# Kernel tuning notes

Hardware: AMD Instinct MI355X
Metric: run time of the kernel (lower is better)

The kernel has to match this reference:

```python
import jax, jax.numpy as jnp
import numpy as np

WS = (7, 7, 7)          # window size (s, h, w)
N_TOK = WS[0] * WS[1] * WS[2]   # 343
DIM = 96
HEADS = 3
N_WINDOWS = 64
BATCH = 8
B_ = BATCH * N_WINDOWS  # 512


def _rel_pos_index(ws):
    s, h, w = ws
    coords = np.stack(np.meshgrid(np.arange(s), np.arange(h), np.arange(w), indexing='ij'))
    cf = coords.reshape(3, -1)                     # [3, N]
    rel = cf[:, :, None] - cf[:, None, :]          # [3, N, N]
    rel = rel.transpose(1, 2, 0).astype(np.int64)  # [N, N, 3]
    rel[..., 0] += s - 1
    rel[..., 1] += h - 1
    rel[..., 2] += w - 1
    rel[..., 0] *= (2 * h - 1) * (2 * w - 1)
    rel[..., 1] *= (2 * w - 1)
    return rel.sum(-1)                             # [N, N] in [0, (2s-1)(2h-1)(2w-1))


def setup_inputs() -> dict:
    key = jax.random.key(0)
    ks = jax.random.split(key, 8)
    table_len = (2 * WS[0] - 1) * (2 * WS[1] - 1) * (2 * WS[2] - 1)  # 2197
    return {
        'x': jax.random.normal(ks[0], (B_, N_TOK, DIM), dtype=jnp.float32),
        'mask': jax.random.normal(ks[1], (N_WINDOWS, N_TOK, N_TOK), dtype=jnp.float32),
        'qkv_w': jax.random.normal(ks[2], (3 * DIM, DIM), dtype=jnp.float32) * 0.02,
        'qkv_b': jax.random.normal(ks[3], (3 * DIM,), dtype=jnp.float32) * 0.02,
        'proj_w': jax.random.normal(ks[4], (DIM, DIM), dtype=jnp.float32) * 0.02,
        'proj_b': jax.random.normal(ks[5], (DIM,), dtype=jnp.float32) * 0.02,
        'rpb_table': jax.random.normal(ks[6], (table_len, HEADS), dtype=jnp.float32) * 0.02,
        'rel_index': jnp.asarray(_rel_pos_index(WS), dtype=jnp.int32),
    }


def reference(x, mask, qkv_w, qkv_b, proj_w, proj_b, rpb_table, rel_index):
    B, N, C = x.shape
    H = rpb_table.shape[1]
    hd = C // H
    scale = hd ** -0.5

    qkv = x @ qkv_w.T + qkv_b                         # [B, N, 3C]
    qkv = qkv.reshape(B, N, 3, H, hd).transpose(2, 0, 3, 1, 4)  # [3, B, H, N, hd]
    q, k, v = qkv[0] * scale, qkv[1], qkv[2]

    attn = jnp.einsum('bhnd,bhmd->bhnm', q, k)        # [B, H, N, N]
    bias = rpb_table[rel_index].transpose(2, 0, 1)    # [H, N, N]
    attn = attn + bias[None]

    nW = mask.shape[0]
    attn = attn.reshape(B // nW, nW, H, N, N) + mask[None, :, None]
    attn = jax.nn.softmax(attn.reshape(B, H, N, N), axis=-1)

    out = jnp.einsum('bhnm,bhmd->bnhd', attn, v).reshape(B, N, C)
    return out @ proj_w.T + proj_b
```

## Files before the change

### kernel.cpp

```cpp
#include <hip/hip_runtime.h>
#include <stdint.h>

#define NTOK 343
#define L2E 1.4426950408889634f
#define SCALE (0.17677669529663687f * 1.4426950408889634f)

typedef uint32_t u32a __attribute__((may_alias));
typedef __attribute__((ext_vector_type(8))) short short8;
typedef short8 bfrag __attribute__((may_alias));
typedef __attribute__((ext_vector_type(4))) float f32x4;
typedef f32x4 f32x4a __attribute__((may_alias));
typedef __attribute__((ext_vector_type(2))) uint32_t u32x2;
typedef u32x2 u32x2a __attribute__((may_alias));

static __device__ __forceinline__ uint16_t f2bf(float f) {
    uint32_t u = __float_as_uint(f);
    u += 0x7fffu + ((u >> 16) & 1u);
    return (uint16_t)(u >> 16);
}
static __device__ __forceinline__ float bflo(uint32_t p) { return __uint_as_float(p << 16); }
static __device__ __forceinline__ float bfhi(uint32_t p) { return __uint_as_float(p & 0xffff0000u); }

static __device__ __forceinline__ float exp2_fast(float x) {
    float r;
    __asm__("v_exp_f32 %0, %1" : "=v"(r) : "v"(x));
    return r;
}
static __device__ __forceinline__ uint32_t cvtpk_bf16(float lo, float hi) {
    uint32_t r;
    __asm__("v_cvt_pk_bf16_f32 %0, %1, %2" : "=v"(r) : "v"(lo), "v"(hi));
    return r;
}

union abits { uint32_t u[4]; bfrag f; };

__global__ __launch_bounds__(256) void comb_pre(const float* __restrict__ mask,
                                                const float* __restrict__ rpb,
                                                const int* __restrict__ rel,
                                                u32a* __restrict__ comb) {
    int e = blockIdx.x * 256 + threadIdx.x;
    const int total = 64 * NTOK * 176;
    if (e >= total) return;
    int m16 = e & 15;
    int tp = (e >> 4) % 11;
    int rest = e / 176;
    int i = rest % NTOK;
    int w = rest / NTOK;
    int j0 = tp * 32 + m16;
    int j1 = j0 + 16;
    const float* mrow = mask + ((size_t)w * NTOK + i) * NTOK;
    const int* rrow = rel + i * NTOK;
    float mk0 = mrow[j0];
    int r0 = rrow[j0] * 3;
    const bool ok1 = (j1 < NTOK);
    float mk1 = ok1 ? mrow[j1] : 0.f;
    int r1 = ok1 ? rrow[j1] * 3 : 0;
    u32a* cbase = comb + ((size_t)(w * 3) * NTOK + i) * 176 + tp * 16 + m16;
    #pragma unroll
    for (int h = 0; h < 3; ++h) {
        float c0 = (mk0 + rpb[r0 + h]) * L2E;
        uint32_t hi = 0xFF80u;
        if (ok1) hi = (uint32_t)f2bf((mk1 + rpb[r1 + h]) * L2E);
        cbase[(size_t)h * (NTOK * 176)] = (uint32_t)f2bf(c0) | (hi << 16);
    }
}

__global__ __launch_bounds__(256, 2) void qkv_kernel(
    const float* __restrict__ x, const float* __restrict__ qkv_w,
    const float* __restrict__ qkv_b,
    uint16_t* __restrict__ q_ws, uint16_t* __restrict__ k_ws, uint16_t* __restrict__ v_ws)
{
    __shared__ uint16_t w_l[288 * 104];
    __shared__ __align__(16) float bias_l[288];
    const int tid = threadIdx.x;

    {
        f32x4 tmp[27];
        #pragma unroll
        for (int i = 0; i < 27; ++i)
            tmp[i] = ((const f32x4a*)qkv_w)[tid + i * 256];
        for (int e = tid; e < 288; e += 256) {
            float bb = qkv_b[e];
            bias_l[e] = (e < 96) ? bb * SCALE : bb;
        }
        #pragma unroll
        for (int i = 0; i < 27; ++i) {
            int c4 = tid + i * 256;
            int c = c4 / 24, k = (c4 - c * 24) * 4;
            f32x4 v = tmp[i];
            float s = (c < 96) ? SCALE : 1.f;
            uint32_t lo = cvtpk_bf16(v[0] * s, v[1] * s);
            uint32_t hi = cvtpk_bf16(v[2] * s, v[3] * s);
            u32x2 pk = {lo, hi};
            *(u32x2a*)(w_l + c * 104 + k) = pk;
        }
    }
    __syncthreads();

    const int lane = tid & 63, wv4 = tid >> 6;
    const int m = lane & 15, quad = lane >> 4;

    f32x4 bs4[18];
    #pragma unroll
    for (int ct = 0; ct < 18; ++ct)
        bs4[ct] = *(const f32x4*)(bias_l + ct * 16 + 4 * quad);

    uint16_t* const dsts[3] = {q_ws, k_ws, v_ws};
    const int rowbase_blk = blockIdx.x * 256;

    for (int it = 0; it < 4; ++it) {
        const int rowbase = rowbase_blk + (wv4 * 4 + it) * 16;
        const int row = rowbase + m;
        const float* xr = x + (size_t)row * 96;
        abits A[3];
        #pragma unroll
        for (int ch = 0; ch < 3; ++ch) {
            f32x4 a0 = *(const f32x4a*)(xr + ch * 32 + quad * 8);
            f32x4 a1 = *(const f32x4a*)(xr + ch * 32 + quad * 8 + 4);
            A[ch].u[0] = cvtpk_bf16(a0[0], a0[1]);
            A[ch].u[1] = cvtpk_bf16(a0[2], a0[3]);
            A[ch].u[2] = cvtpk_bf16(a1[0], a1[1]);
            A[ch].u[3] = cvtpk_bf16(a1[2], a1[3]);
        }

        f32x4 C[18];
        #pragma unroll
        for (int ct = 0; ct < 18; ++ct) C[ct] = (f32x4){0.f, 0.f, 0.f, 0.f};

        #pragma unroll
        for (int ch = 0; ch < 3; ++ch) {
            #pragma unroll
            for (int ct = 0; ct < 18; ++ct) {
                bfrag bf_ = *(const bfrag*)(w_l + (ct * 16 + m) * 104 + ch * 32 + quad * 8);
                C[ct] = __builtin_amdgcn_mfma_f32_16x16x32_bf16(bf_, A[ch].f, C[ct], 0, 0, 0);
            }
        }

        const int bb = row / 343;
        const int nn = row - bb * 343;
        #pragma unroll
        for (int ct = 0; ct < 18; ++ct) {
            const int sel = ct / 6;
            const int base = (ct % 6) * 16 + 4 * quad;
            const int hd = base >> 5, dd = base & 31;
            f32x4 vv = C[ct] + bs4[ct];
            uint32_t lo = cvtpk_bf16(vv[0], vv[1]);
            uint32_t hi = cvtpk_bf16(vv[2], vv[3]);
            uint16_t* dp_ = dsts[sel] + ((size_t)(bb * 3 + hd) * NTOK + nn) * 32 + dd;
            u32x2 pk = {lo, hi};
            *(u32x2a*)dp_ = pk;
        }
    }
}

__global__ __launch_bounds__(256, 2) void attn_kernel(
    uint16_t* __restrict__ q_ws, const uint16_t* __restrict__ k_ws,
    const uint16_t* __restrict__ v_ws, const u32a* __restrict__ comb)
{
    __shared__ uint16_t k_l[352 * 40];
    __shared__ uint16_t vT[32 * 360];
    __shared__ uint16_t pstage[4][16 * 104];

    const int bh = blockIdx.x;
    const int b = bh / 3, h = bh - b * 3, w = b & 63;
    const int tid = threadIdx.x, lane = tid & 63, wv = tid >> 6;
    const int m = lane & 15, quad = lane >> 4;
    const int wh = w * 3 + h;

    const u32a* ksrc = (const u32a*)(k_ws + (size_t)bh * NTOK * 32);
    const u32a* vsrc = (const u32a*)(v_ws + (size_t)bh * NTOK * 32);
    u32a* k32 = (u32a*)k_l;
    {
        uint32_t tk[22], tv[22];
        #pragma unroll
        for (int i = 0; i < 22; ++i) {
            int e = tid + i * 256;
            if (e < NTOK * 16) { tk[i] = ksrc[e]; tv[i] = vsrc[e]; }
        }
        #pragma unroll
        for (int i = 0; i < 22; ++i) {
            int e = tid + i * 256;
            if (e < NTOK * 16) {
                int tok = e >> 4, dp = e & 15;
                k32[tok * 20 + dp] = tk[i];
                uint32_t vv = tv[i];
                int kp = ((tok >> 5) << 5) + ((tok & 15) << 1) + ((tok >> 4) & 1);
                vT[(2 * dp) * 360 + kp]     = (uint16_t)(vv & 0xffffu);
                vT[(2 * dp + 1) * 360 + kp] = (uint16_t)(vv >> 16);
            }
        }
    }
    for (int e = tid; e < 9 * 16; e += 256) {
        int tok = 343 + (e >> 4), dp = e & 15;
        k32[tok * 20 + dp] = 0;
    }
    for (int e = tid; e < 32 * 9; e += 256) {
        int d = e / 9, tok = 343 + (e % 9);
        int kp = ((tok >> 5) << 5) + ((tok & 15) << 1) + ((tok >> 4) & 1);
        vT[d * 360 + kp] = 0;
    }
    __syncthreads();

    uint16_t* qbase = q_ws + (size_t)bh * NTOK * 32;
    uint16_t* stg = pstage[wv];

    for (int ti = wv; ti < 22; ti += 4) {
        const int i0 = ti * 16;
        bfrag qf = *(const bfrag*)(qbase + (size_t)(i0 + m) * 32 + quad * 8);
        uint32_t cw[4][11];
        #pragma unroll
        for (int r = 0; r < 4; ++r) {
            int ir = i0 + 4 * quad + r;
            ir = (ir > 342) ? 342 : ir;
            const u32a* crow = comb + ((size_t)(wh * NTOK + ir)) * 176 + m;
            #pragma unroll
            for (int tp = 0; tp < 11; ++tp)
                cw[r][tp] = crow[tp * 16];
        }

        f32x4 S[22];
        #pragma unroll
        for (int t = 0; t < 22; ++t) S[t] = (f32x4){0.f, 0.f, 0.f, 0.f};
        __builtin_amdgcn_s_setprio(1);
        #pragma unroll
        for (int t = 0; t < 22; ++t) {
            bfrag kf = *(const bfrag*)(k_l + (t * 16 + m) * 40 + quad * 8);
            S[t] = __builtin_amdgcn_mfma_f32_16x16x32_bf16(qf, kf, S[t], 0, 0, 0);
        }
        __builtin_amdgcn_s_setprio(0);

        float sum[4] = {0.f, 0.f, 0.f, 0.f};

        f32x4 O0 = (f32x4){0.f, 0.f, 0.f, 0.f};
        f32x4 O1 = (f32x4){0.f, 0.f, 0.f, 0.f};
        #pragma unroll
        for (int qt = 0; qt < 4; ++qt) {
            const int nch = (qt == 3) ? 2 : 3;
            #pragma unroll
            for (int uu = 0; uu < 3; ++uu) {
                if (uu < nch) {
                    const int tp = qt * 3 + uu;
                    #pragma unroll
                    for (int r = 0; r < 4; ++r) {
                        float e0 = exp2_fast(S[2 * tp][r] + bflo(cw[r][tp]));
                        float e1 = exp2_fast(S[2 * tp + 1][r] + bfhi(cw[r][tp]));
                        sum[r] += e0 + e1;
                        *(u32a*)(stg + (4 * quad + r) * 104 + uu * 32 + 2 * m) =
                            cvtpk_bf16(e0, e1);
                    }
                }
            }
            __asm__ __volatile__("" ::: "memory");
            __builtin_amdgcn_s_waitcnt(0xC07F);
            __asm__ __volatile__("" ::: "memory");

            __builtin_amdgcn_s_setprio(1);
            #pragma unroll
            for (int c = 0; c < 3; ++c) {
                if (c < nch) {
                    const int jj = qt * 96 + c * 32;
                    bfrag pf = *(const bfrag*)(stg + m * 104 + c * 32 + quad * 8);
                    bfrag v0 = *(const bfrag*)(vT + (size_t)m * 360 + jj + quad * 8);
                    bfrag v1 = *(const bfrag*)(vT + (size_t)(m + 16) * 360 + jj + quad * 8);
                    O0 = __builtin_amdgcn_mfma_f32_16x16x32_bf16(pf, v0, O0, 0, 0, 0);
                    O1 = __builtin_amdgcn_mfma_f32_16x16x32_bf16(pf, v1, O1, 0, 0, 0);
                }
            }
            __builtin_amdgcn_s_setprio(0);
            __asm__ __volatile__("" ::: "memory");
        }

        float inv_[4];
        #pragma unroll
        for (int r = 0; r < 4; ++r) {
            float v = sum[r];
            v += __shfl_xor(v, 1);
            v += __shfl_xor(v, 2);
            v += __shfl_xor(v, 4);
            v += __shfl_xor(v, 8);
            inv_[r] = 1.f / v;
        }

        #pragma unroll
        for (int r = 0; r < 4; ++r) {
            const int ir = i0 + 4 * quad + r;
            if (ir < NTOK) {
                uint16_t* orow = qbase + (size_t)ir * 32;
                orow[m]      = f2bf(O0[r] * inv_[r]);
                orow[m + 16] = f2bf(O1[r] * inv_[r]);
            }
        }
    }
}

__global__ __launch_bounds__(256) void proj_kernel(
    const uint16_t* __restrict__ ao, const float* __restrict__ proj_w,
    const float* __restrict__ proj_b, float* __restrict__ out)
{
    __shared__ uint16_t w_l[96 * 104];
    const int tid = threadIdx.x;
    {
        f32x4 tmp[9];
        #pragma unroll
        for (int i = 0; i < 9; ++i)
            tmp[i] = ((const f32x4a*)proj_w)[tid + i * 256];
        #pragma unroll
        for (int i = 0; i < 9; ++i) {
            int c4 = tid + i * 256;
            int c = c4 / 24, k = (c4 - c * 24) * 4;
            f32x4 v = tmp[i];
            uint32_t lo = cvtpk_bf16(v[0], v[1]);
            uint32_t hi = cvtpk_bf16(v[2], v[3]);
            u32x2 pk = {lo, hi};
            *(u32x2a*)(w_l + c * 104 + k) = pk;
        }
    }
    __syncthreads();

    const int lane = tid & 63, wv4 = tid >> 6;
    const int m = lane & 15, quad = lane >> 4;

    float bp[6];
    #pragma unroll
    for (int ct = 0; ct < 6; ++ct) bp[ct] = proj_b[ct * 16 + m];

    const int rowbase_blk = blockIdx.x * 256;

    for (int it = 0; it < 4; ++it) {
        const int rowbase = rowbase_blk + (wv4 * 4 + it) * 16;
        const int rm = rowbase + m;
        const int bm = rm / 343;
        const int nm = rm - bm * 343;

        f32x4 C[6];
        #pragma unroll
        for (int ct = 0; ct < 6; ++ct) C[ct] = (f32x4){0.f, 0.f, 0.f, 0.f};

        #pragma unroll
        for (int ch = 0; ch < 3; ++ch) {
            bfrag af = *(const bfrag*)(ao + ((size_t)(bm * 3 + ch) * NTOK + nm) * 32 + quad * 8);
            #pragma unroll
            for (int ct = 0; ct < 6; ++ct) {
                bfrag bf_ = *(const bfrag*)(w_l + (ct * 16 + m) * 104 + ch * 32 + quad * 8);
                C[ct] = __builtin_amdgcn_mfma_f32_16x16x32_bf16(af, bf_, C[ct], 0, 0, 0);
            }
        }

        #pragma unroll
        for (int r = 0; r < 4; ++r) {
            const int rr = rowbase + 4 * quad + r;
            #pragma unroll
            for (int ct = 0; ct < 6; ++ct)
                out[(size_t)rr * 96 + ct * 16 + m] = C[ct][r] + bp[ct];
        }
    }
}

extern "C" void kernel_launch(void* const* d_in, const int* in_sizes, int n_in,
                              void* d_out, int out_size, void* d_ws, size_t ws_size,
                              hipStream_t stream) {
    const float* x      = (const float*)d_in[0];
    const float* mask   = (const float*)d_in[1];
    const float* qkv_w  = (const float*)d_in[2];
    const float* qkv_b  = (const float*)d_in[3];
    const float* proj_w = (const float*)d_in[4];
    const float* proj_b = (const float*)d_in[5];
    const float* rpb    = (const float*)d_in[6];
    const int*   rel    = (const int*)d_in[7];
    float* out = (float*)d_out;

    uint16_t* q_ws = (uint16_t*)d_ws;
    uint16_t* k_ws = q_ws + 16859136;
    uint16_t* v_ws = k_ws + 16859136;
    u32a* comb = (u32a*)((char*)d_ws + 101154816);

    const int comb_total = 64 * NTOK * 176;
    comb_pre<<<dim3((comb_total + 255) / 256), 256, 0, stream>>>(mask, rpb, rel, comb);
    qkv_kernel<<<dim3(686), 256, 0, stream>>>(x, qkv_w, qkv_b, q_ws, k_ws, v_ws);
    attn_kernel<<<dim3(512 * 3), 256, 0, stream>>>(q_ws, k_ws, v_ws, comb);
    proj_kernel<<<dim3(686), 256, 0, stream>>>(q_ws, proj_w, proj_b, out);
}
```

Measured before the change: 330.3 us.

## Restructure QKV and projection GEMM kernels for load prefetch and fewer accumulators

```diff
diff --git a/kernel.cpp b/kernel.cpp
--- a/kernel.cpp
+++ b/kernel.cpp
@@ -65,7 +65,55 @@
     }
 }
 
-__global__ __launch_bounds__(256, 2) void qkv_kernel(
+#define QKV_LOADX(DST, ROW) do { \
+    const float* xr_ = x + (size_t)(ROW) * 96 + quad * 8; \
+    DST##0 = *(const f32x4a*)(xr_); \
+    DST##1 = *(const f32x4a*)(xr_ + 4); \
+    DST##2 = *(const f32x4a*)(xr_ + 32); \
+    DST##3 = *(const f32x4a*)(xr_ + 36); \
+    DST##4 = *(const f32x4a*)(xr_ + 64); \
+    DST##5 = *(const f32x4a*)(xr_ + 68); \
+} while (0)
+
+#define QKV_COMPUTE(SRC, ITC) do { \
+    abits A0_, A1_, A2_; \
+    A0_.u[0] = cvtpk_bf16(SRC##0[0], SRC##0[1]); \
+    A0_.u[1] = cvtpk_bf16(SRC##0[2], SRC##0[3]); \
+    A0_.u[2] = cvtpk_bf16(SRC##1[0], SRC##1[1]); \
+    A0_.u[3] = cvtpk_bf16(SRC##1[2], SRC##1[3]); \
+    A1_.u[0] = cvtpk_bf16(SRC##2[0], SRC##2[1]); \
+    A1_.u[1] = cvtpk_bf16(SRC##2[2], SRC##2[3]); \
+    A1_.u[2] = cvtpk_bf16(SRC##3[0], SRC##3[1]); \
+    A1_.u[3] = cvtpk_bf16(SRC##3[2], SRC##3[3]); \
+    A2_.u[0] = cvtpk_bf16(SRC##4[0], SRC##4[1]); \
+    A2_.u[1] = cvtpk_bf16(SRC##4[2], SRC##4[3]); \
+    A2_.u[2] = cvtpk_bf16(SRC##5[0], SRC##5[1]); \
+    A2_.u[3] = cvtpk_bf16(SRC##5[2], SRC##5[3]); \
+    const int rowc = row0 + (ITC) * 16; \
+    const int bbc = rowc / 343; \
+    const int nnc = rowc - bbc * 343; \
+    _Pragma("unroll") \
+    for (int ct = 0; ct < 18; ++ct) { \
+        f32x4 Cl = (f32x4){0.f, 0.f, 0.f, 0.f}; \
+        bfrag w0_ = *(const bfrag*)(w_l + (ct * 16 + m) * 104 + quad * 8); \
+        Cl = __builtin_amdgcn_mfma_f32_16x16x32_bf16(w0_, A0_.f, Cl, 0, 0, 0); \
+        bfrag w1_ = *(const bfrag*)(w_l + (ct * 16 + m) * 104 + 32 + quad * 8); \
+        Cl = __builtin_amdgcn_mfma_f32_16x16x32_bf16(w1_, A1_.f, Cl, 0, 0, 0); \
+        bfrag w2_ = *(const bfrag*)(w_l + (ct * 16 + m) * 104 + 64 + quad * 8); \
+        Cl = __builtin_amdgcn_mfma_f32_16x16x32_bf16(w2_, A2_.f, Cl, 0, 0, 0); \
+        f32x4 b4_ = *(const f32x4*)(bias_l + ct * 16 + 4 * quad); \
+        f32x4 vv_ = Cl + b4_; \
+        const int sel_ = ct / 6; \
+        const int base_ = (ct % 6) * 16 + 4 * quad; \
+        const int hd_ = base_ >> 5, dd_ = base_ & 31; \
+        uint32_t lo_ = cvtpk_bf16(vv_[0], vv_[1]); \
+        uint32_t hi_ = cvtpk_bf16(vv_[2], vv_[3]); \
+        u32x2 pk_ = {lo_, hi_}; \
+        *(u32x2a*)(dsts[sel_] + ((size_t)(bbc * 3 + hd_) * NTOK + nnc) * 32 + dd_) = pk_; \
+    } \
+} while (0)
+
+__global__ __launch_bounds__(512, 4) void qkv_kernel(
     const float* __restrict__ x, const float* __restrict__ qkv_w,
     const float* __restrict__ qkv_b,
     uint16_t* __restrict__ q_ws, uint16_t* __restrict__ k_ws, uint16_t* __restrict__ v_ws)
@@ -75,82 +123,44 @@
     const int tid = threadIdx.x;
 
     {
-        f32x4 tmp[27];
-        #pragma unroll
-        for (int i = 0; i < 27; ++i)
-            tmp[i] = ((const f32x4a*)qkv_w)[tid + i * 256];
-        for (int e = tid; e < 288; e += 256) {
+        f32x4 tmp[14];
+        #pragma unroll
+        for (int i = 0; i < 14; ++i) {
+            int idx = tid + i * 512;
+            if (idx < 6912) tmp[i] = ((const f32x4a*)qkv_w)[idx];
+        }
+        for (int e = tid; e < 288; e += 512) {
             float bb = qkv_b[e];
             bias_l[e] = (e < 96) ? bb * SCALE : bb;
         }
         #pragma unroll
-        for (int i = 0; i < 27; ++i) {
-            int c4 = tid + i * 256;
-            int c = c4 / 24, k = (c4 - c * 24) * 4;
-            f32x4 v = tmp[i];
-            float s = (c < 96) ? SCALE : 1.f;
-            uint32_t lo = cvtpk_bf16(v[0] * s, v[1] * s);
-            uint32_t hi = cvtpk_bf16(v[2] * s, v[3] * s);
-            u32x2 pk = {lo, hi};
-            *(u32x2a*)(w_l + c * 104 + k) = pk;
+        for (int i = 0; i < 14; ++i) {
+            int idx = tid + i * 512;
+            if (idx < 6912) {
+                int c = idx / 24, k = (idx - c * 24) * 4;
+                f32x4 v = tmp[i];
+                float s = (c < 96) ? SCALE : 1.f;
+                uint32_t lo = cvtpk_bf16(v[0] * s, v[1] * s);
+                uint32_t hi = cvtpk_bf16(v[2] * s, v[3] * s);
+                u32x2 pk = {lo, hi};
+                *(u32x2a*)(w_l + c * 104 + k) = pk;
+            }
         }
     }
     __syncthreads();
 
-    const int lane = tid & 63, wv4 = tid >> 6;
+    const int lane = tid & 63, wv8 = tid >> 6;
     const int m = lane & 15, quad = lane >> 4;
 
-    f32x4 bs4[18];
-    #pragma unroll
-    for (int ct = 0; ct < 18; ++ct)
-        bs4[ct] = *(const f32x4*)(bias_l + ct * 16 + 4 * quad);
-
     uint16_t* const dsts[3] = {q_ws, k_ws, v_ws};
-    const int rowbase_blk = blockIdx.x * 256;
-
-    for (int it = 0; it < 4; ++it) {
-        const int rowbase = rowbase_blk + (wv4 * 4 + it) * 16;
-        const int row = rowbase + m;
-        const float* xr = x + (size_t)row * 96;
-        abits A[3];
-        #pragma unroll
-        for (int ch = 0; ch < 3; ++ch) {
-            f32x4 a0 = *(const f32x4a*)(xr + ch * 32 + quad * 8);
-            f32x4 a1 = *(const f32x4a*)(xr + ch * 32 + quad * 8 + 4);
-            A[ch].u[0] = cvtpk_bf16(a0[0], a0[1]);
-            A[ch].u[1] = cvtpk_bf16(a0[2], a0[3]);
-            A[ch].u[2] = cvtpk_bf16(a1[0], a1[1]);
-            A[ch].u[3] = cvtpk_bf16(a1[2], a1[3]);
-        }
-
-        f32x4 C[18];
-        #pragma unroll
-        for (int ct = 0; ct < 18; ++ct) C[ct] = (f32x4){0.f, 0.f, 0.f, 0.f};
-
-        #pragma unroll
-        for (int ch = 0; ch < 3; ++ch) {
-            #pragma unroll
-            for (int ct = 0; ct < 18; ++ct) {
-                bfrag bf_ = *(const bfrag*)(w_l + (ct * 16 + m) * 104 + ch * 32 + quad * 8);
-                C[ct] = __builtin_amdgcn_mfma_f32_16x16x32_bf16(bf_, A[ch].f, C[ct], 0, 0, 0);
-            }
-        }
-
-        const int bb = row / 343;
-        const int nn = row - bb * 343;
-        #pragma unroll
-        for (int ct = 0; ct < 18; ++ct) {
-            const int sel = ct / 6;
-            const int base = (ct % 6) * 16 + 4 * quad;
-            const int hd = base >> 5, dd = base & 31;
-            f32x4 vv = C[ct] + bs4[ct];
-            uint32_t lo = cvtpk_bf16(vv[0], vv[1]);
-            uint32_t hi = cvtpk_bf16(vv[2], vv[3]);
-            uint16_t* dp_ = dsts[sel] + ((size_t)(bb * 3 + hd) * NTOK + nn) * 32 + dd;
-            u32x2 pk = {lo, hi};
-            *(u32x2a*)dp_ = pk;
-        }
-    }
+    const int row0 = blockIdx.x * 256 + wv8 * 32 + m;
+
+    f32x4 tA0, tA1, tA2, tA3, tA4, tA5;
+    f32x4 tB0, tB1, tB2, tB3, tB4, tB5;
+    QKV_LOADX(tA, row0);
+    QKV_LOADX(tB, row0 + 16);
+    QKV_COMPUTE(tA, 0);
+    QKV_COMPUTE(tB, 1);
 }
 
 __global__ __launch_bounds__(256, 2) void attn_kernel(
@@ -293,6 +303,30 @@
     }
 }
 
+#define PROJ_LOADA(DST, RM) do { \
+    const int bm_ = (RM) / 343; \
+    const int nm_ = (RM) - bm_ * 343; \
+    const uint16_t* ab_ = ao + ((size_t)(bm_ * 3) * NTOK + nm_) * 32 + quad * 8; \
+    DST##0 = *(const bfrag*)(ab_); \
+    DST##1 = *(const bfrag*)(ab_ + (size_t)NTOK * 32); \
+    DST##2 = *(const bfrag*)(ab_ + (size_t)(2 * NTOK) * 32); \
+} while (0)
+
+#define PROJ_COMPUTE(SRC, ITC) do { \
+    float* orow_ = out + (size_t)(row0 + (ITC) * 16) * 96 + 4 * quad; \
+    _Pragma("unroll") \
+    for (int ct = 0; ct < 6; ++ct) { \
+        f32x4 Cl = (f32x4){0.f, 0.f, 0.f, 0.f}; \
+        bfrag w0_ = *(const bfrag*)(w_l + (ct * 16 + m) * 104 + quad * 8); \
+        Cl = __builtin_amdgcn_mfma_f32_16x16x32_bf16(w0_, SRC##0, Cl, 0, 0, 0); \
+        bfrag w1_ = *(const bfrag*)(w_l + (ct * 16 + m) * 104 + 32 + quad * 8); \
+        Cl = __builtin_amdgcn_mfma_f32_16x16x32_bf16(w1_, SRC##1, Cl, 0, 0, 0); \
+        bfrag w2_ = *(const bfrag*)(w_l + (ct * 16 + m) * 104 + 64 + quad * 8); \
+        Cl = __builtin_amdgcn_mfma_f32_16x16x32_bf16(w2_, SRC##2, Cl, 0, 0, 0); \
+        *(f32x4a*)(orow_ + ct * 16) = Cl + bp4[ct]; \
+    } \
+} while (0)
+
 __global__ __launch_bounds__(256) void proj_kernel(
     const uint16_t* __restrict__ ao, const float* __restrict__ proj_w,
     const float* __restrict__ proj_b, float* __restrict__ out)
@@ -320,40 +354,22 @@
     const int lane = tid & 63, wv4 = tid >> 6;
     const int m = lane & 15, quad = lane >> 4;
 
-    float bp[6];
+    f32x4 bp4[6];
     #pragma unroll
-    for (int ct = 0; ct < 6; ++ct) bp[ct] = proj_b[ct * 16 + m];
-
-    const int rowbase_blk = blockIdx.x * 256;
-
-    for (int it = 0; it < 4; ++it) {
-        const int rowbase = rowbase_blk + (wv4 * 4 + it) * 16;
-        const int rm = rowbase + m;
-        const int bm = rm / 343;
-        const int nm = rm - bm * 343;
-
-        f32x4 C[6];
-        #pragma unroll
-        for (int ct = 0; ct < 6; ++ct) C[ct] = (f32x4){0.f, 0.f, 0.f, 0.f};
-
-        #pragma unroll
-        for (int ch = 0; ch < 3; ++ch) {
-            bfrag af = *(const bfrag*)(ao + ((size_t)(bm * 3 + ch) * NTOK + nm) * 32 + quad * 8);
-            #pragma unroll
-            for (int ct = 0; ct < 6; ++ct) {
-                bfrag bf_ = *(const bfrag*)(w_l + (ct * 16 + m) * 104 + ch * 32 + quad * 8);
-                C[ct] = __builtin_amdgcn_mfma_f32_16x16x32_bf16(af, bf_, C[ct], 0, 0, 0);
-            }
-        }
-
-        #pragma unroll
-        for (int r = 0; r < 4; ++r) {
-            const int rr = rowbase + 4 * quad + r;
-            #pragma unroll
-            for (int ct = 0; ct < 6; ++ct)
-                out[(size_t)rr * 96 + ct * 16 + m] = C[ct][r] + bp[ct];
-        }
-    }
+    for (int ct = 0; ct < 6; ++ct)
+        bp4[ct] = *(const f32x4a*)(proj_b + ct * 16 + 4 * quad);
+
+    const int row0 = blockIdx.x * 256 + wv4 * 64 + m;
+
+    bfrag aA0, aA1, aA2, aB0, aB1, aB2;
+    PROJ_LOADA(aA, row0);
+    PROJ_LOADA(aB, row0 + 16);
+    PROJ_COMPUTE(aA, 0);
+    PROJ_LOADA(aA, row0 + 32);
+    PROJ_COMPUTE(aB, 1);
+    PROJ_LOADA(aB, row0 + 48);
+    PROJ_COMPUTE(aA, 2);
+    PROJ_COMPUTE(aB, 3);
 }
 
 extern "C" void kernel_launch(void* const* d_in, const int* in_sizes, int n_in,
@@ -376,7 +392,7 @@
 
     const int comb_total = 64 * NTOK * 176;
     comb_pre<<<dim3((comb_total + 255) / 256), 256, 0, stream>>>(mask, rpb, rel, comb);
-    qkv_kernel<<<dim3(686), 256, 0, stream>>>(x, qkv_w, qkv_b, q_ws, k_ws, v_ws);
+    qkv_kernel<<<dim3(686), 512, 0, stream>>>(x, qkv_w, qkv_b, q_ws, k_ws, v_ws);
     attn_kernel<<<dim3(512 * 3), 256, 0, stream>>>(q_ws, k_ws, v_ws, comb);
     proj_kernel<<<dim3(686), 256, 0, stream>>>(q_ws, proj_w, proj_b, out);
 }
```

Measured after the change: 288.1 us. 12.8% less time.
